# Optimization experiments

Hardware: AMD Instinct MI355X
Metric: run time of the kernel (lower is better)

The kernel has to match this reference:

```python
import jax, jax.numpy as jnp
import numpy as np

N0, N1, N2 = 200000, 600000, 400000
NNZ1, NNZ2 = 1200000, 1200000
G = 256          # number of graphs in the batch
H = 128          # num_hidden
NIN = 32         # num_input
L = 2            # num_layers
R = 3            # max_rank + 1


def setup_inputs() -> dict:
    key = jax.random.key(0)
    ks = jax.random.split(key, 24)
    d = {}
    d["x0"] = jax.random.normal(ks[0], (N0, NIN), jnp.float32)
    d["x1"] = jax.random.normal(ks[1], (N1, NIN), jnp.float32)
    d["x2"] = jax.random.normal(ks[2], (N2, NIN), jnp.float32)
    d["b1_rows"] = jax.random.randint(ks[3], (NNZ1,), 0, N0, jnp.int32)
    d["b1_cols"] = jax.random.randint(ks[4], (NNZ1,), 0, N1, jnp.int32)
    d["b2_rows"] = jax.random.randint(ks[5], (NNZ2,), 0, N1, jnp.int32)
    d["b2_cols"] = jax.random.randint(ks[6], (NNZ2,), 0, N2, jnp.int32)
    d["batch0"] = jnp.sort(jax.random.randint(ks[7], (N0,), 0, G, jnp.int32))
    d["batch1"] = jnp.sort(jax.random.randint(ks[8], (N1,), 0, G, jnp.int32))
    d["batch2"] = jnp.sort(jax.random.randint(ks[9], (N2,), 0, G, jnp.int32))
    sin = 1.0 / np.sqrt(NIN).astype(np.float32)
    sh = 1.0 / np.sqrt(H).astype(np.float32)
    d["w_emb"] = jax.random.normal(ks[10], (NIN, H), jnp.float32) * sin
    d["b_emb"] = jnp.zeros((H,), jnp.float32)
    # one conv weight per (layer, rank>0): message W for B_r^T @ (x @ W)
    d["conv_w"] = jax.random.normal(ks[11], (L, 2, H, H), jnp.float32) * sh
    d["pre_w1"] = jax.random.normal(ks[12], (R, H, H), jnp.float32) * sh
    d["pre_b1"] = jnp.zeros((R, H), jnp.float32)
    d["pre_w2"] = jax.random.normal(ks[13], (R, H, H), jnp.float32) * sh
    d["pre_b2"] = jnp.zeros((R, H), jnp.float32)
    d["post_w1"] = jax.random.normal(ks[14], (R * H, H), jnp.float32) * (1.0 / np.sqrt(R * H).astype(np.float32))
    d["post_b1"] = jnp.zeros((H,), jnp.float32)
    d["post_w2"] = jax.random.normal(ks[15], (H, 1), jnp.float32) * sh
    d["post_b2"] = jnp.zeros((1,), jnp.float32)
    return d


def reference(x0, x1, x2, b1_rows, b1_cols, b2_rows, b2_cols,
              batch0, batch1, batch2,
              w_emb, b_emb, conv_w,
              pre_w1, pre_b1, pre_w2, pre_b2,
              post_w1, post_b1, post_w2, post_b2):
    # feature embedding (shared across ranks)
    h0 = x0 @ w_emb + b_emb
    h1 = x1 @ w_emb + b_emb
    h2 = x2 @ w_emb + b_emb

    for l in range(L):
        # sparse incidence matmul B_r^T @ h_{r-1}: gather rows, scatter-add to cols
        m1 = jax.ops.segment_sum(h0[b1_rows], b1_cols, num_segments=N1)
        m2 = jax.ops.segment_sum(h1[b2_rows], b2_cols, num_segments=N2)
        # aggregation with sigmoid update; rank 0 has no incoming messages
        h0 = jax.nn.sigmoid(h0)
        h1 = jax.nn.sigmoid(m1 @ conv_w[l, 0])
        h2 = jax.nn.sigmoid(m2 @ conv_w[l, 1])

    def pre_pool(h, r):
        z = jax.nn.silu(h @ pre_w1[r] + pre_b1[r])
        return z @ pre_w2[r] + pre_b2[r]

    # global_add_pool per rank -> [G, H] each
    p0 = jax.ops.segment_sum(pre_pool(h0, 0), batch0, num_segments=G)
    p1 = jax.ops.segment_sum(pre_pool(h1, 1), batch1, num_segments=G)
    p2 = jax.ops.segment_sum(pre_pool(h2, 2), batch2, num_segments=G)

    state = jnp.concatenate([p0, p1, p2], axis=1)  # [G, 3H]
    z = jax.nn.silu(state @ post_w1 + post_b1)
    out = z @ post_w2 + post_b2                     # [G, 1]
    return jnp.squeeze(out, axis=-1)                # [G]
```

## Files before the change

### kernel.cpp

```cpp
#include <hip/hip_runtime.h>
#include <math.h>

#define HDIM 128
#define NIN_ 32
#define RANKS 3

typedef unsigned int u32;
typedef unsigned short u16;
typedef __attribute__((ext_vector_type(8))) short short8;
typedef __attribute__((ext_vector_type(8))) __bf16 bf16x8;
typedef __attribute__((ext_vector_type(4))) float f32x4;

__device__ __forceinline__ float bf2f(u16 b) { return __uint_as_float(((u32)b) << 16); }
__device__ __forceinline__ u16 f2bf(float f) {
    u32 u = __float_as_uint(f);
    u32 r = u + 0x7fffu + ((u >> 16) & 1u);
    return (u16)(r >> 16);
}
__device__ __forceinline__ float sigmoidf_(float x) {
    return __builtin_amdgcn_rcpf(1.0f + __builtin_amdgcn_exp2f(-1.44269504f * x));
}
__device__ __forceinline__ float siluf_(float x) { return x * sigmoidf_(x); }

template <int SIG>
__device__ __forceinline__ float sigpow(float f) {
#pragma unroll
    for (int q = 0; q < SIG; ++q) f = sigmoidf_(f);
    return f;
}

__global__ void zero_kernel(u32* __restrict__ p, long long nw) {
    long long i = (long long)blockIdx.x * blockDim.x + threadIdx.x;
    long long stride = (long long)gridDim.x * blockDim.x;
    for (; i < nw; i += stride) p[i] = 0u;
}

__global__ void count_kernel(const int* __restrict__ cols, int* __restrict__ cnt, int nnz) {
    int e = blockIdx.x * 256 + threadIdx.x;
    if (e < nnz) atomicAdd(&cnt[cols[e]], 1);
}

__global__ void scan1_kernel(const int* __restrict__ cnt, int* __restrict__ bsum, int ndst) {
    __shared__ int lds[256];
    int base = blockIdx.x * 1024, t = threadIdx.x;
    int s = 0;
#pragma unroll
    for (int j = 0; j < 4; ++j) {
        int i = base + t * 4 + j;
        s += (i < ndst) ? cnt[i] : 0;
    }
    lds[t] = s;
    __syncthreads();
    for (int off = 128; off > 0; off >>= 1) {
        if (t < off) lds[t] += lds[t + off];
        __syncthreads();
    }
    if (t == 0) bsum[blockIdx.x] = lds[0];
}

__global__ void scan2_kernel(int* __restrict__ bsum, int nb, int* __restrict__ total) {
    __shared__ int lds[256];
    int t = threadIdx.x;
    int v[8];
    int s = 0;
#pragma unroll
    for (int j = 0; j < 8; ++j) {
        int i = t * 8 + j;
        v[j] = (i < nb) ? bsum[i] : 0;
        s += v[j];
    }
    lds[t] = s;
    __syncthreads();
    for (int off = 1; off < 256; off <<= 1) {
        int y = (t >= off) ? lds[t - off] : 0;
        __syncthreads();
        lds[t] += y;
        __syncthreads();
    }
    int run = lds[t] - s;
#pragma unroll
    for (int j = 0; j < 8; ++j) {
        int i = t * 8 + j;
        if (i < nb) {
            bsum[i] = run;
            run += v[j];
        }
    }
    if (t == 255) *total = run;
}

__global__ void scan3_kernel(const int* __restrict__ cnt, const int* __restrict__ bsum,
                             int* __restrict__ rowptr, int* __restrict__ cursor, int ndst) {
    __shared__ int lds[256];
    int base = blockIdx.x * 1024, t = threadIdx.x;
    int v[4];
    int s = 0;
#pragma unroll
    for (int j = 0; j < 4; ++j) {
        int i = base + t * 4 + j;
        v[j] = (i < ndst) ? cnt[i] : 0;
        s += v[j];
    }
    lds[t] = s;
    __syncthreads();
    for (int off = 1; off < 256; off <<= 1) {
        int y = (t >= off) ? lds[t - off] : 0;
        __syncthreads();
        lds[t] += y;
        __syncthreads();
    }
    int run = bsum[blockIdx.x] + lds[t] - s;
#pragma unroll
    for (int j = 0; j < 4; ++j) {
        int i = base + t * 4 + j;
        if (i < ndst) {
            rowptr[i] = run;
            cursor[i] = run;
            run += v[j];
        }
    }
}

__global__ void fill_kernel(const int* __restrict__ rows, const int* __restrict__ cols,
                            int* __restrict__ cursor, int* __restrict__ esrc, int nnz) {
    int e = blockIdx.x * 256 + threadIdx.x;
    if (e >= nnz) return;
    int idx = atomicAdd(&cursor[cols[e]], 1);
    esrc[idx] = rows[e];
}

__global__ void wprep_kernel(const float* __restrict__ conv_w, const float* __restrict__ pre_w1,
                             const float* __restrict__ pre_w2, u16* __restrict__ wt, int Lnum) {
    int tid = blockIdx.x * 256 + threadIdx.x;
    int nm = 2 * Lnum + 6;
    if (tid >= nm * 128 * 128) return;
    int m = tid >> 14;
    int r = tid & 16383;
    int k = r >> 7;
    int col = r & 127;
    const float* src;
    if (m < 2 * Lnum) src = conv_w + (size_t)m * 16384;
    else if (m < 2 * Lnum + 3) src = pre_w1 + (size_t)(m - 2 * Lnum) * 16384;
    else src = pre_w2 + (size_t)(m - 2 * Lnum - 3) * 16384;
    float v = src[k * 128 + col];
    wt[(size_t)m * 16384 + col * 128 + (k ^ ((col & 7) << 3))] = f2bf(v);
}

__global__ void wembprep_kernel(const float* __restrict__ w_emb, u16* __restrict__ wembT) {
    int tid = blockIdx.x * 256 + threadIdx.x;
    if (tid >= HDIM * NIN_) return;
    int col = tid >> 5, k = tid & 31;
    wembT[col * 32 + k] = f2bf(w_emb[k * HDIM + col]);
}

__global__ __launch_bounds__(512) void embed_mfma_kernel(const float* __restrict__ x,
                                                         const u16* __restrict__ wembT,
                                                         const float* __restrict__ b,
                                                         u16* __restrict__ h, int n) {
    __shared__ u16 cs[8][16][128];
    const int tid = threadIdx.x;
    const int wave = tid >> 6, lane = tid & 63;
    const int row0 = blockIdx.x * 128;
    const int col = lane & 15, kg = lane >> 4;
    const int wrow0 = row0 + wave * 16;
    const int arow = wrow0 + col;
    const int arowc = arow < n ? arow : (n - 1);

    bf16x8 afrag;
    {
        const float4* xp = (const float4*)(x + (size_t)arowc * NIN_ + kg * 8);
        float4 xa = xp[0], xb = xp[1];
        short8 s;
        s[0] = (short)f2bf(xa.x); s[1] = (short)f2bf(xa.y);
        s[2] = (short)f2bf(xa.z); s[3] = (short)f2bf(xa.w);
        s[4] = (short)f2bf(xb.x); s[5] = (short)f2bf(xb.y);
        s[6] = (short)f2bf(xb.z); s[7] = (short)f2bf(xb.w);
        afrag = __builtin_bit_cast(bf16x8, s);
    }

#pragma unroll
    for (int ct = 0; ct < 8; ++ct) {
        int bcol = ct * 16 + col;
        bf16x8 bfrag = *(const bf16x8*)(wembT + bcol * 32 + kg * 8);
        f32x4 acc = (f32x4){0.f, 0.f, 0.f, 0.f};
        acc = __builtin_amdgcn_mfma_f32_16x16x32_bf16(afrag, bfrag, acc, 0, 0, 0);
        float bv = b[bcol];
#pragma unroll
        for (int r = 0; r < 4; ++r) {
            int crow = kg * 4 + r;
            cs[wave][crow][(ct * 16 + col) ^ ((crow & 7) << 3)] = f2bf(acc[r] + bv);
        }
    }
#pragma unroll
    for (int it = 0; it < 4; ++it) {
        int cid = it * 64 + lane;
        int r = cid >> 4, c = cid & 15;
        int grow = wrow0 + r;
        if (grow < n) {
            short8 v = *(const short8*)(&cs[wave][r][(c * 8) ^ ((r & 7) << 3)]);
            *(short8*)(h + (size_t)grow * HDIM + c * 8) = v;
        }
    }
}

__device__ __forceinline__ void gemm128(const bf16x8 afrag[4], const u16* wls, f32x4 acc[8],
                                        int col, int kg) {
#pragma unroll
    for (int ct = 0; ct < 8; ++ct) {
        int bcol = ct * 16 + col;
        const u16* bb = wls + bcol * 128;
        int swz = (bcol & 7) << 3;
#pragma unroll
        for (int k0 = 0; k0 < 4; ++k0) {
            bf16x8 bfrag = *(const bf16x8*)(bb + ((k0 * 32 + kg * 8) ^ swz));
            acc[ct] = __builtin_amdgcn_mfma_f32_16x16x32_bf16(afrag[k0], bfrag, acc[ct], 0, 0, 0);
        }
    }
}

__device__ __forceinline__ void stage_w(const u16* __restrict__ w, u16* wls, int tid) {
    const uint4* g = (const uint4*)w;
    uint4* l = (uint4*)wls;
    for (int i = tid; i < 2048; i += 512) l[i] = g[i];
}

__device__ __forceinline__ void pool_acc(const f32x4 acc[8], const float* __restrict__ b2,
                                         const int* __restrict__ batch, float* __restrict__ p,
                                         int n, int colOff, int wrow0, int col, int kg) {
    if (wrow0 >= n) return;
    int rend = wrow0 + 15 < n ? wrow0 + 15 : (n - 1);
    int bstart = batch[wrow0];
    int bend = batch[rend];
    if (bstart == bend) {
#pragma unroll
        for (int ct = 0; ct < 8; ++ct) {
            float b2v = b2[ct * 16 + col];
            float s = 0.f;
#pragma unroll
            for (int r = 0; r < 4; ++r) {
                int row = wrow0 + kg * 4 + r;
                if (row < n) s += acc[ct][r] + b2v;
            }
            s += __shfl_xor(s, 16, 64);
            s += __shfl_xor(s, 32, 64);
            if (kg == 0) atomicAdd(&p[bstart * (RANKS * HDIM) + colOff + ct * 16 + col], s);
        }
    } else {
        int bgs[4];
#pragma unroll
        for (int r = 0; r < 4; ++r) {
            int row = wrow0 + kg * 4 + r;
            bgs[r] = (row < n) ? batch[row] : -1;
        }
#pragma unroll
        for (int ct = 0; ct < 8; ++ct) {
            float b2v = b2[ct * 16 + col];
            int curb = -1;
            float cur = 0.f;
#pragma unroll
            for (int r = 0; r < 4; ++r) {
                if (bgs[r] >= 0) {
                    if (bgs[r] != curb) {
                        if (curb >= 0)
                            atomicAdd(&p[curb * (RANKS * HDIM) + colOff + ct * 16 + col], cur);
                        curb = bgs[r];
                        cur = 0.f;
                    }
                    cur += acc[ct][r] + b2v;
                }
            }
            if (curb >= 0) atomicAdd(&p[curb * (RANKS * HDIM) + colOff + ct * 16 + col], cur);
        }
    }
}

template <int MODE, int SIG>
__global__ __launch_bounds__(512) void fused_mfma_kernel(
    const u16* __restrict__ srcbuf, const int* __restrict__ rowptr,
    const int* __restrict__ esrc, const u16* __restrict__ wconv,
    const u16* __restrict__ w1t, const u16* __restrict__ w2t,
    const float* __restrict__ b1, const float* __restrict__ b2,
    const int* __restrict__ batch, float* __restrict__ p, int colOff,
    u16* __restrict__ outB, int n) {
    __shared__ u16 wls[16384];
    __shared__ u16 zs[8][16][128];
    const int tid = threadIdx.x;
    const int wave = tid >> 6, lane = tid & 63;
    const int row0 = blockIdx.x * 128;
    const int col = lane & 15, kg = lane >> 4;
    const int wrow0 = row0 + wave * 16;

    stage_w(wconv, wls, tid);

    float ga[4][8];
#pragma unroll
    for (int k0 = 0; k0 < 4; ++k0)
#pragma unroll
        for (int j = 0; j < 8; ++j) ga[k0][j] = 0.f;
    const int arow = wrow0 + col;
    if (arow < n) {
        int beg = rowptr[arow], end = rowptr[arow + 1];
        for (int e = beg; e < end; e += 2) {
            int s0 = esrc[e];
            bool has1 = (e + 1 < end);
            int s1 = has1 ? esrc[e + 1] : s0;
            const bf16x8* p0 = (const bf16x8*)(srcbuf + (size_t)s0 * HDIM + kg * 8);
            const bf16x8* p1 = (const bf16x8*)(srcbuf + (size_t)s1 * HDIM + kg * 8);
            bf16x8 v0[4], v1[4];
#pragma unroll
            for (int k0 = 0; k0 < 4; ++k0) { v0[k0] = p0[k0 * 4]; v1[k0] = p1[k0 * 4]; }
#pragma unroll
            for (int k0 = 0; k0 < 4; ++k0) {
                short8 sv = __builtin_bit_cast(short8, v0[k0]);
#pragma unroll
                for (int j = 0; j < 8; ++j) ga[k0][j] += sigpow<SIG>(bf2f((u16)sv[j]));
            }
            if (has1) {
#pragma unroll
                for (int k0 = 0; k0 < 4; ++k0) {
                    short8 sv = __builtin_bit_cast(short8, v1[k0]);
#pragma unroll
                    for (int j = 0; j < 8; ++j) ga[k0][j] += sigpow<SIG>(bf2f((u16)sv[j]));
                }
            }
        }
    }
    bf16x8 afrag[4];
#pragma unroll
    for (int k0 = 0; k0 < 4; ++k0) {
        short8 s;
#pragma unroll
        for (int j = 0; j < 8; ++j) s[j] = (short)f2bf(ga[k0][j]);
        afrag[k0] = __builtin_bit_cast(bf16x8, s);
    }
    __syncthreads();

    f32x4 acc[8];
#pragma unroll
    for (int ct = 0; ct < 8; ++ct) acc[ct] = (f32x4){0.f, 0.f, 0.f, 0.f};
    gemm128(afrag, wls, acc, col, kg);

#pragma unroll
    for (int ct = 0; ct < 8; ++ct)
#pragma unroll
        for (int r = 0; r < 4; ++r) {
            int crow = kg * 4 + r;
            zs[wave][crow][(ct * 16 + col) ^ ((crow & 7) << 3)] = f2bf(sigmoidf_(acc[ct][r]));
        }

    if (MODE == 0) {
#pragma unroll
        for (int it = 0; it < 4; ++it) {
            int cid = it * 64 + lane;
            int r = cid >> 4, c = cid & 15;
            int grow = wrow0 + r;
            if (grow < n) {
                short8 v = *(const short8*)(&zs[wave][r][(c * 8) ^ ((r & 7) << 3)]);
                *(short8*)(outB + (size_t)grow * HDIM + c * 8) = v;
            }
        }
        return;
    }

    __syncthreads();
    stage_w(w1t, wls, tid);
    __syncthreads();

    bf16x8 zfrag[4];
    {
        int zswz = (col & 7) << 3;
#pragma unroll
        for (int k0 = 0; k0 < 4; ++k0)
            zfrag[k0] = *(const bf16x8*)(&zs[wave][col][(k0 * 32 + kg * 8) ^ zswz]);
    }
#pragma unroll
    for (int ct = 0; ct < 8; ++ct) acc[ct] = (f32x4){0.f, 0.f, 0.f, 0.f};
    gemm128(zfrag, wls, acc, col, kg);
#pragma unroll
    for (int ct = 0; ct < 8; ++ct) {
        float b1v = b1[ct * 16 + col];
#pragma unroll
        for (int r = 0; r < 4; ++r) {
            int crow = kg * 4 + r;
            zs[wave][crow][(ct * 16 + col) ^ ((crow & 7) << 3)] = f2bf(siluf_(acc[ct][r] + b1v));
        }
    }
    __syncthreads();
    stage_w(w2t, wls, tid);
    __syncthreads();

    {
        int zswz = (col & 7) << 3;
#pragma unroll
        for (int k0 = 0; k0 < 4; ++k0)
            zfrag[k0] = *(const bf16x8*)(&zs[wave][col][(k0 * 32 + kg * 8) ^ zswz]);
    }
#pragma unroll
    for (int ct = 0; ct < 8; ++ct) acc[ct] = (f32x4){0.f, 0.f, 0.f, 0.f};
    gemm128(zfrag, wls, acc, col, kg);

    pool_acc(acc, b2, batch, p, n, colOff, wrow0, col, kg);
}

template <int SIG>
__global__ __launch_bounds__(512) void prepool_mfma_kernel(
    const u16* __restrict__ h, const u16* __restrict__ w1t, const u16* __restrict__ w2t,
    const float* __restrict__ b1, const float* __restrict__ b2, const int* __restrict__ batch,
    float* __restrict__ p, int n, int colOff) {
    __shared__ u16 wls[16384];
    __shared__ u16 zs[8][16][128];
    const int tid = threadIdx.x;
    const int wave = tid >> 6, lane = tid & 63;
    const int row0 = blockIdx.x * 128;
    const int col = lane & 15, kg = lane >> 4;
    const int wrow0 = row0 + wave * 16;

    stage_w(w1t, wls, tid);

    const int arow = wrow0 + col;
    const int arowc = arow < n ? arow : (n - 1);
    bf16x8 afrag[4];
    {
        const bf16x8* ap = (const bf16x8*)(h + (size_t)arowc * HDIM + kg * 8);
#pragma unroll
        for (int k0 = 0; k0 < 4; ++k0) afrag[k0] = ap[k0 * 4];
    }
    if (SIG > 0) {
#pragma unroll
        for (int k0 = 0; k0 < 4; ++k0) {
            short8 s = __builtin_bit_cast(short8, afrag[k0]);
#pragma unroll
            for (int j = 0; j < 8; ++j) s[j] = (short)f2bf(sigpow<SIG>(bf2f((u16)s[j])));
            afrag[k0] = __builtin_bit_cast(bf16x8, s);
        }
    }
    __syncthreads();

    f32x4 acc[8];
#pragma unroll
    for (int ct = 0; ct < 8; ++ct) acc[ct] = (f32x4){0.f, 0.f, 0.f, 0.f};
    gemm128(afrag, wls, acc, col, kg);
#pragma unroll
    for (int ct = 0; ct < 8; ++ct) {
        float b1v = b1[ct * 16 + col];
#pragma unroll
        for (int r = 0; r < 4; ++r) {
            int crow = kg * 4 + r;
            zs[wave][crow][(ct * 16 + col) ^ ((crow & 7) << 3)] = f2bf(siluf_(acc[ct][r] + b1v));
        }
    }
    __syncthreads();
    stage_w(w2t, wls, tid);
    __syncthreads();

    bf16x8 zfrag[4];
    {
        int zswz = (col & 7) << 3;
#pragma unroll
        for (int k0 = 0; k0 < 4; ++k0)
            zfrag[k0] = *(const bf16x8*)(&zs[wave][col][(k0 * 32 + kg * 8) ^ zswz]);
    }
#pragma unroll
    for (int ct = 0; ct < 8; ++ct) acc[ct] = (f32x4){0.f, 0.f, 0.f, 0.f};
    gemm128(zfrag, wls, acc, col, kg);

    pool_acc(acc, b2, batch, p, n, colOff, wrow0, col, kg);
}

__global__ void final_kernel(const float* __restrict__ p, const float* __restrict__ w1,
                             const float* __restrict__ b1, const float* __restrict__ w2,
                             const float* __restrict__ b2, float* __restrict__ out) {
    const int g = blockIdx.x;
    const int c = threadIdx.x;
    const float* pg = p + g * (RANKS * HDIM);
    float acc = b1[c];
    for (int k = 0; k < RANKS * HDIM; ++k) acc = fmaf(pg[k], w1[k * HDIM + c], acc);
    float z = siluf_(acc);
    float v = z * w2[c];
#pragma unroll
    for (int off = 32; off > 0; off >>= 1) v += __shfl_down(v, off, 64);
    __shared__ float red[2];
    if ((c & 63) == 0) red[c >> 6] = v;
    __syncthreads();
    if (c == 0) out[g] = red[0] + red[1] + b2[0];
}

#define LAUNCH_FUSED(MODE, SIG_, grid, ...)                                       \
    fused_mfma_kernel<MODE, SIG_><<<grid, 512, 0, stream>>>(__VA_ARGS__)

static inline void launch_fused0(int sig, int grid, hipStream_t stream,
                                 const u16* src, const int* rp, const int* es, const u16* wc,
                                 u16* outB, int n) {
    switch (sig) {
        case 0: LAUNCH_FUSED(0, 0, grid, src, rp, es, wc, nullptr, nullptr, nullptr, nullptr, nullptr, nullptr, 0, outB, n); break;
        case 1: LAUNCH_FUSED(0, 1, grid, src, rp, es, wc, nullptr, nullptr, nullptr, nullptr, nullptr, nullptr, 0, outB, n); break;
        case 2: LAUNCH_FUSED(0, 2, grid, src, rp, es, wc, nullptr, nullptr, nullptr, nullptr, nullptr, nullptr, 0, outB, n); break;
        default: LAUNCH_FUSED(0, 3, grid, src, rp, es, wc, nullptr, nullptr, nullptr, nullptr, nullptr, nullptr, 0, outB, n); break;
    }
}

static inline void launch_fused1(int sig, int grid, hipStream_t stream,
                                 const u16* src, const int* rp, const int* es, const u16* wc,
                                 const u16* w1t, const u16* w2t, const float* b1, const float* b2,
                                 const int* batch, float* p, int colOff, int n) {
    switch (sig) {
        case 0: LAUNCH_FUSED(1, 0, grid, src, rp, es, wc, w1t, w2t, b1, b2, batch, p, colOff, nullptr, n); break;
        case 1: LAUNCH_FUSED(1, 1, grid, src, rp, es, wc, w1t, w2t, b1, b2, batch, p, colOff, nullptr, n); break;
        case 2: LAUNCH_FUSED(1, 2, grid, src, rp, es, wc, w1t, w2t, b1, b2, batch, p, colOff, nullptr, n); break;
        default: LAUNCH_FUSED(1, 3, grid, src, rp, es, wc, w1t, w2t, b1, b2, batch, p, colOff, nullptr, n); break;
    }
}

extern "C" void kernel_launch(void* const* d_in, const int* in_sizes, int n_in,
                              void* d_out, int out_size, void* d_ws, size_t ws_size,
                              hipStream_t stream) {
    const float* x0 = (const float*)d_in[0];
    const float* x1 = (const float*)d_in[1];
    const int* b1_rows = (const int*)d_in[3];
    const int* b1_cols = (const int*)d_in[4];
    const int* b2_rows = (const int*)d_in[5];
    const int* b2_cols = (const int*)d_in[6];
    const int* batch0 = (const int*)d_in[7];
    const int* batch1 = (const int*)d_in[8];
    const int* batch2 = (const int*)d_in[9];
    const float* w_emb = (const float*)d_in[10];
    const float* b_emb = (const float*)d_in[11];
    const float* conv_w = (const float*)d_in[12];
    const float* pre_w1 = (const float*)d_in[13];
    const float* pre_b1 = (const float*)d_in[14];
    const float* pre_w2 = (const float*)d_in[15];
    const float* pre_b2 = (const float*)d_in[16];
    const float* post_w1 = (const float*)d_in[17];
    const float* post_b1 = (const float*)d_in[18];
    const float* post_w2 = (const float*)d_in[19];
    const float* post_b2 = (const float*)d_in[20];

    const int N0 = in_sizes[0] / NIN_;
    const int N1 = in_sizes[1] / NIN_;
    const int N2 = in_sizes[2] / NIN_;
    const int NNZ1 = in_sizes[3];
    const int NNZ2 = in_sizes[5];
    const int L = in_sizes[12] / (2 * HDIM * HDIM);
    const int Gn = out_size;

    u16* A = (u16*)d_ws;
    u16* B = A + (size_t)N0 * HDIM;
    float* p = (float*)(B + (size_t)N1 * HDIM);
    u16* wt = (u16*)(p + (size_t)Gn * RANKS * HDIM);
    const u16* wt_conv = wt;
    const u16* wt_p1 = wt + (size_t)2 * L * 16384;
    const u16* wt_p2 = wt_p1 + (size_t)3 * 16384;
    u16* wembT = wt + (size_t)(2 * L + 6) * 16384;
    int* ip = (int*)(wembT + 4096);
    int* rowptr1 = ip;  ip += N1 + 1;
    int* rowptr2 = ip;  ip += N2 + 1;
    int* esrc1 = ip;    ip += NNZ1;
    int* esrc2 = ip;    ip += NNZ2;
    int maxN = N1 > N2 ? N1 : N2;
    int* cnt = ip;      ip += maxN;
    int* cursor = ip;   ip += maxN;
    int* bsum = ip;     ip += 2048;

    {
        int tot = (2 * L + 6) * 16384;
        wprep_kernel<<<(tot + 255) / 256, 256, 0, stream>>>(conv_w, pre_w1, pre_w2, wt, L);
        wembprep_kernel<<<16, 256, 0, stream>>>(w_emb, wembT);

        zero_kernel<<<512, 256, 0, stream>>>((u32*)cnt, N1);
        count_kernel<<<(NNZ1 + 255) / 256, 256, 0, stream>>>(b1_cols, cnt, NNZ1);
        int nb1 = (N1 + 1023) / 1024;
        scan1_kernel<<<nb1, 256, 0, stream>>>(cnt, bsum, N1);
        scan2_kernel<<<1, 256, 0, stream>>>(bsum, nb1, rowptr1 + N1);
        scan3_kernel<<<nb1, 256, 0, stream>>>(cnt, bsum, rowptr1, cursor, N1);
        fill_kernel<<<(NNZ1 + 255) / 256, 256, 0, stream>>>(b1_rows, b1_cols, cursor, esrc1, NNZ1);

        zero_kernel<<<512, 256, 0, stream>>>((u32*)cnt, N2);
        count_kernel<<<(NNZ2 + 255) / 256, 256, 0, stream>>>(b2_cols, cnt, NNZ2);
        int nb2 = (N2 + 1023) / 1024;
        scan1_kernel<<<nb2, 256, 0, stream>>>(cnt, bsum, N2);
        scan2_kernel<<<1, 256, 0, stream>>>(bsum, nb2, rowptr2 + N2);
        scan3_kernel<<<nb2, 256, 0, stream>>>(cnt, bsum, rowptr2, cursor, N2);
        fill_kernel<<<(NNZ2 + 255) / 256, 256, 0, stream>>>(b2_rows, b2_cols, cursor, esrc2, NNZ2);
    }

    embed_mfma_kernel<<<(N0 + 127) / 128, 512, 0, stream>>>(x0, wembT, b_emb, A, N0);

    zero_kernel<<<64, 256, 0, stream>>>((u32*)p, (long long)Gn * RANKS * HDIM);

    if (L >= 2) {
        launch_fused0(L - 2, (N1 + 127) / 128, stream, A, rowptr1, esrc1,
                      wt_conv + (size_t)((L - 2) * 2 + 0) * 16384, B, N1);
    } else {
        embed_mfma_kernel<<<(N1 + 127) / 128, 512, 0, stream>>>(x1, wembT, b_emb, B, N1);
    }

    launch_fused1(0, (N2 + 127) / 128, stream, B, rowptr2, esrc2,
                  wt_conv + (size_t)((L - 1) * 2 + 1) * 16384,
                  wt_p1 + 2 * 16384, wt_p2 + 2 * 16384, pre_b1 + 2 * HDIM, pre_b2 + 2 * HDIM,
                  batch2, p, 2 * HDIM, N2);

    launch_fused1(L - 1, (N1 + 127) / 128, stream, A, rowptr1, esrc1,
                  wt_conv + (size_t)((L - 1) * 2 + 0) * 16384,
                  wt_p1 + 1 * 16384, wt_p2 + 1 * 16384, pre_b1 + 1 * HDIM, pre_b2 + 1 * HDIM,
                  batch1, p, 1 * HDIM, N1);

    {
        int grid = (N0 + 127) / 128;
        switch (L) {
            case 1: prepool_mfma_kernel<1><<<grid, 512, 0, stream>>>(
                        A, wt_p1, wt_p2, pre_b1, pre_b2, batch0, p, N0, 0); break;
            case 2: prepool_mfma_kernel<2><<<grid, 512, 0, stream>>>(
                        A, wt_p1, wt_p2, pre_b1, pre_b2, batch0, p, N0, 0); break;
            default: prepool_mfma_kernel<3><<<grid, 512, 0, stream>>>(
                        A, wt_p1, wt_p2, pre_b1, pre_b2, batch0, p, N0, 0); break;
        }
    }

    final_kernel<<<Gn, HDIM, 0, stream>>>(p, post_w1, post_b1, post_w2, post_b2, (float*)d_out);
}
```

Before: 855.8 us.

## Merge both rank-1 conv layers into one kernel sharing a single gather

```diff
diff --git a/kernel.cpp b/kernel.cpp
--- a/kernel.cpp
+++ b/kernel.cpp
@@ -274,6 +274,156 @@
     }
 }
 
+template <int SIGA>
+__global__ __launch_bounds__(512) void merged_n1_kernel(
+    const u16* __restrict__ srcbuf, const int* __restrict__ rowptr,
+    const int* __restrict__ esrc, const u16* __restrict__ wc0, const u16* __restrict__ wc1,
+    const u16* __restrict__ w1t, const u16* __restrict__ w2t,
+    const float* __restrict__ b1, const float* __restrict__ b2,
+    const int* __restrict__ batch, float* __restrict__ p, int colOff,
+    u16* __restrict__ outB, int n) {
+    __shared__ u16 wls[16384];
+    __shared__ u16 zs[8][16][128];
+    const int tid = threadIdx.x;
+    const int wave = tid >> 6, lane = tid & 63;
+    const int row0 = blockIdx.x * 128;
+    const int col = lane & 15, kg = lane >> 4;
+    const int wrow0 = row0 + wave * 16;
+
+    stage_w(wc0, wls, tid);
+
+    float gr[4][8], gs[4][8];
+#pragma unroll
+    for (int k0 = 0; k0 < 4; ++k0)
+#pragma unroll
+        for (int j = 0; j < 8; ++j) { gr[k0][j] = 0.f; gs[k0][j] = 0.f; }
+
+    const int arow = wrow0 + col;
+    if (arow < n) {
+        int beg = rowptr[arow], end = rowptr[arow + 1];
+        for (int e = beg; e < end; e += 2) {
+            int s0 = esrc[e];
+            bool has1 = (e + 1 < end);
+            int s1 = has1 ? esrc[e + 1] : s0;
+            const bf16x8* p0 = (const bf16x8*)(srcbuf + (size_t)s0 * HDIM + kg * 8);
+            const bf16x8* p1 = (const bf16x8*)(srcbuf + (size_t)s1 * HDIM + kg * 8);
+            bf16x8 v0[4], v1[4];
+#pragma unroll
+            for (int k0 = 0; k0 < 4; ++k0) { v0[k0] = p0[k0 * 4]; v1[k0] = p1[k0 * 4]; }
+#pragma unroll
+            for (int k0 = 0; k0 < 4; ++k0) {
+                short8 sv = __builtin_bit_cast(short8, v0[k0]);
+#pragma unroll
+                for (int j = 0; j < 8; ++j) {
+                    float f = sigpow<SIGA>(bf2f((u16)sv[j]));
+                    gr[k0][j] += f;
+                    gs[k0][j] += sigmoidf_(f);
+                }
+            }
+            if (has1) {
+#pragma unroll
+                for (int k0 = 0; k0 < 4; ++k0) {
+                    short8 sv = __builtin_bit_cast(short8, v1[k0]);
+#pragma unroll
+                    for (int j = 0; j < 8; ++j) {
+                        float f = sigpow<SIGA>(bf2f((u16)sv[j]));
+                        gr[k0][j] += f;
+                        gs[k0][j] += sigmoidf_(f);
+                    }
+                }
+            }
+        }
+    }
+    bf16x8 afragR[4], afragS[4];
+#pragma unroll
+    for (int k0 = 0; k0 < 4; ++k0) {
+        short8 sR, sS;
+#pragma unroll
+        for (int j = 0; j < 8; ++j) {
+            sR[j] = (short)f2bf(gr[k0][j]);
+            sS[j] = (short)f2bf(gs[k0][j]);
+        }
+        afragR[k0] = __builtin_bit_cast(bf16x8, sR);
+        afragS[k0] = __builtin_bit_cast(bf16x8, sS);
+    }
+    __syncthreads();
+
+    f32x4 acc[8];
+#pragma unroll
+    for (int ct = 0; ct < 8; ++ct) acc[ct] = (f32x4){0.f, 0.f, 0.f, 0.f};
+    gemm128(afragR, wls, acc, col, kg);
+#pragma unroll
+    for (int ct = 0; ct < 8; ++ct)
+#pragma unroll
+        for (int r = 0; r < 4; ++r) {
+            int crow = kg * 4 + r;
+            zs[wave][crow][(ct * 16 + col) ^ ((crow & 7) << 3)] = f2bf(sigmoidf_(acc[ct][r]));
+        }
+#pragma unroll
+    for (int it = 0; it < 4; ++it) {
+        int cid = it * 64 + lane;
+        int r = cid >> 4, c = cid & 15;
+        int grow = wrow0 + r;
+        if (grow < n) {
+            short8 v = *(const short8*)(&zs[wave][r][(c * 8) ^ ((r & 7) << 3)]);
+            *(short8*)(outB + (size_t)grow * HDIM + c * 8) = v;
+        }
+    }
+
+    __syncthreads();
+    stage_w(wc1, wls, tid);
+    __syncthreads();
+
+#pragma unroll
+    for (int ct = 0; ct < 8; ++ct) acc[ct] = (f32x4){0.f, 0.f, 0.f, 0.f};
+    gemm128(afragS, wls, acc, col, kg);
+#pragma unroll
+    for (int ct = 0; ct < 8; ++ct)
+#pragma unroll
+        for (int r = 0; r < 4; ++r) {
+            int crow = kg * 4 + r;
+            zs[wave][crow][(ct * 16 + col) ^ ((crow & 7) << 3)] = f2bf(sigmoidf_(acc[ct][r]));
+        }
+    __syncthreads();
+    stage_w(w1t, wls, tid);
+    __syncthreads();
+
+    bf16x8 zfrag[4];
+    {
+        int zswz = (col & 7) << 3;
+#pragma unroll
+        for (int k0 = 0; k0 < 4; ++k0)
+            zfrag[k0] = *(const bf16x8*)(&zs[wave][col][(k0 * 32 + kg * 8) ^ zswz]);
+    }
+#pragma unroll
+    for (int ct = 0; ct < 8; ++ct) acc[ct] = (f32x4){0.f, 0.f, 0.f, 0.f};
+    gemm128(zfrag, wls, acc, col, kg);
+#pragma unroll
+    for (int ct = 0; ct < 8; ++ct) {
+        float b1v = b1[ct * 16 + col];
+#pragma unroll
+        for (int r = 0; r < 4; ++r) {
+            int crow = kg * 4 + r;
+            zs[wave][crow][(ct * 16 + col) ^ ((crow & 7) << 3)] = f2bf(siluf_(acc[ct][r] + b1v));
+        }
+    }
+    __syncthreads();
+    stage_w(w2t, wls, tid);
+    __syncthreads();
+
+    {
+        int zswz = (col & 7) << 3;
+#pragma unroll
+        for (int k0 = 0; k0 < 4; ++k0)
+            zfrag[k0] = *(const bf16x8*)(&zs[wave][col][(k0 * 32 + kg * 8) ^ zswz]);
+    }
+#pragma unroll
+    for (int ct = 0; ct < 8; ++ct) acc[ct] = (f32x4){0.f, 0.f, 0.f, 0.f};
+    gemm128(zfrag, wls, acc, col, kg);
+
+    pool_acc(acc, b2, batch, p, n, colOff, wrow0, col, kg);
+}
+
 template <int MODE, int SIG>
 __global__ __launch_bounds__(512) void fused_mfma_kernel(
     const u16* __restrict__ srcbuf, const int* __restrict__ rowptr,
@@ -483,32 +633,6 @@
     if ((c & 63) == 0) red[c >> 6] = v;
     __syncthreads();
     if (c == 0) out[g] = red[0] + red[1] + b2[0];
-}
-
-#define LAUNCH_FUSED(MODE, SIG_, grid, ...)                                       \
-    fused_mfma_kernel<MODE, SIG_><<<grid, 512, 0, stream>>>(__VA_ARGS__)
-
-static inline void launch_fused0(int sig, int grid, hipStream_t stream,
-                                 const u16* src, const int* rp, const int* es, const u16* wc,
-                                 u16* outB, int n) {
-    switch (sig) {
-        case 0: LAUNCH_FUSED(0, 0, grid, src, rp, es, wc, nullptr, nullptr, nullptr, nullptr, nullptr, nullptr, 0, outB, n); break;
-        case 1: LAUNCH_FUSED(0, 1, grid, src, rp, es, wc, nullptr, nullptr, nullptr, nullptr, nullptr, nullptr, 0, outB, n); break;
-        case 2: LAUNCH_FUSED(0, 2, grid, src, rp, es, wc, nullptr, nullptr, nullptr, nullptr, nullptr, nullptr, 0, outB, n); break;
-        default: LAUNCH_FUSED(0, 3, grid, src, rp, es, wc, nullptr, nullptr, nullptr, nullptr, nullptr, nullptr, 0, outB, n); break;
-    }
-}
-
-static inline void launch_fused1(int sig, int grid, hipStream_t stream,
-                                 const u16* src, const int* rp, const int* es, const u16* wc,
-                                 const u16* w1t, const u16* w2t, const float* b1, const float* b2,
-                                 const int* batch, float* p, int colOff, int n) {
-    switch (sig) {
-        case 0: LAUNCH_FUSED(1, 0, grid, src, rp, es, wc, w1t, w2t, b1, b2, batch, p, colOff, nullptr, n); break;
-        case 1: LAUNCH_FUSED(1, 1, grid, src, rp, es, wc, w1t, w2t, b1, b2, batch, p, colOff, nullptr, n); break;
-        case 2: LAUNCH_FUSED(1, 2, grid, src, rp, es, wc, w1t, w2t, b1, b2, batch, p, colOff, nullptr, n); break;
-        default: LAUNCH_FUSED(1, 3, grid, src, rp, es, wc, w1t, w2t, b1, b2, batch, p, colOff, nullptr, n); break;
-    }
 }
 
 extern "C" void kernel_launch(void* const* d_in, const int* in_sizes, int n_in,
@@ -588,21 +712,31 @@
     zero_kernel<<<64, 256, 0, stream>>>((u32*)p, (long long)Gn * RANKS * HDIM);
 
     if (L >= 2) {
-        launch_fused0(L - 2, (N1 + 127) / 128, stream, A, rowptr1, esrc1,
-                      wt_conv + (size_t)((L - 2) * 2 + 0) * 16384, B, N1);
+        int grid = (N1 + 127) / 128;
+        const u16* wc0 = wt_conv + (size_t)((L - 2) * 2 + 0) * 16384;
+        const u16* wc1 = wt_conv + (size_t)((L - 1) * 2 + 0) * 16384;
+        switch (L - 2) {
+            case 0: merged_n1_kernel<0><<<grid, 512, 0, stream>>>(
+                        A, rowptr1, esrc1, wc0, wc1, wt_p1 + 16384, wt_p2 + 16384,
+                        pre_b1 + HDIM, pre_b2 + HDIM, batch1, p, HDIM, B, N1); break;
+            case 1: merged_n1_kernel<1><<<grid, 512, 0, stream>>>(
+                        A, rowptr1, esrc1, wc0, wc1, wt_p1 + 16384, wt_p2 + 16384,
+                        pre_b1 + HDIM, pre_b2 + HDIM, batch1, p, HDIM, B, N1); break;
+            default: merged_n1_kernel<2><<<grid, 512, 0, stream>>>(
+                        A, rowptr1, esrc1, wc0, wc1, wt_p1 + 16384, wt_p2 + 16384,
+                        pre_b1 + HDIM, pre_b2 + HDIM, batch1, p, HDIM, B, N1); break;
+        }
     } else {
         embed_mfma_kernel<<<(N1 + 127) / 128, 512, 0, stream>>>(x1, wembT, b_emb, B, N1);
-    }
-
-    launch_fused1(0, (N2 + 127) / 128, stream, B, rowptr2, esrc2,
-                  wt_conv + (size_t)((L - 1) * 2 + 1) * 16384,
-                  wt_p1 + 2 * 16384, wt_p2 + 2 * 16384, pre_b1 + 2 * HDIM, pre_b2 + 2 * HDIM,
-                  batch2, p, 2 * HDIM, N2);
-
-    launch_fused1(L - 1, (N1 + 127) / 128, stream, A, rowptr1, esrc1,
-                  wt_conv + (size_t)((L - 1) * 2 + 0) * 16384,
-                  wt_p1 + 1 * 16384, wt_p2 + 1 * 16384, pre_b1 + 1 * HDIM, pre_b2 + 1 * HDIM,
-                  batch1, p, 1 * HDIM, N1);
+        fused_mfma_kernel<1, 0><<<(N1 + 127) / 128, 512, 0, stream>>>(
+            A, rowptr1, esrc1, wt_conv, wt_p1 + 16384, wt_p2 + 16384,
+            pre_b1 + HDIM, pre_b2 + HDIM, batch1, p, HDIM, nullptr, N1);
+    }
+
+    fused_mfma_kernel<1, 0><<<(N2 + 127) / 128, 512, 0, stream>>>(
+        B, rowptr2, esrc2, wt_conv + (size_t)((L - 1) * 2 + 1) * 16384,
+        wt_p1 + 2 * 16384, wt_p2 + 2 * 16384, pre_b1 + 2 * HDIM, pre_b2 + 2 * HDIM,
+        batch2, p, 2 * HDIM, nullptr, N2);
 
     {
         int grid = (N0 + 127) / 128;
```

Result: faster. 794.1 us (-7.2%).
